# Kernel optimization log

Measured on AMD Instinct MI355X. Metric: run time of the kernel, lower is better.

Reference implementation:

```python
import jax, jax.numpy as jnp
import numpy as np

N_NODES = 50000
N_EDGES = 640000
D_IN = 128
HIDDEN = 128
OUT = 64


def sage_conv(x, edge_index, W_l, b_l, W_r):
    # PyG SAGEConv (mean aggr): out = lin_l(mean_j x_j) + lin_r(x_i)
    src, dst = edge_index[0], edge_index[1]
    msgs = x[src]                                             # [E, d] gather
    agg = jax.ops.segment_sum(msgs, dst, num_segments=x.shape[0])
    cnt = jax.ops.segment_sum(jnp.ones((edge_index.shape[1],), x.dtype), dst,
                              num_segments=x.shape[0])
    mean = agg / jnp.maximum(cnt, 1.0)[:, None]
    return mean @ W_l.T + b_l + x @ W_r.T


def setup_inputs() -> dict:
    key = jax.random.key(0)
    ks = jax.random.split(key, 8)
    s = lambda d: 1.0 / np.sqrt(d)
    x = jax.random.normal(ks[0], (N_NODES, D_IN), dtype=jnp.float32)
    edge_index = jax.random.randint(ks[1], (2, N_EDGES), 0, N_NODES, dtype=jnp.int64)
    return {
        "x": x,
        "edge_index": edge_index,
        "W1_l": jax.random.normal(ks[2], (HIDDEN, D_IN), jnp.float32) * s(D_IN),
        "b1_l": jnp.zeros((HIDDEN,), jnp.float32),
        "W1_r": jax.random.normal(ks[3], (HIDDEN, D_IN), jnp.float32) * s(D_IN),
        "W2_l": jax.random.normal(ks[4], (HIDDEN, HIDDEN), jnp.float32) * s(HIDDEN),
        "b2_l": jnp.zeros((HIDDEN,), jnp.float32),
        "W2_r": jax.random.normal(ks[5], (HIDDEN, HIDDEN), jnp.float32) * s(HIDDEN),
        "W3": jax.random.normal(ks[6], (OUT, HIDDEN), jnp.float32) * s(HIDDEN),
        "b3": jnp.zeros((OUT,), jnp.float32),
    }


def reference(x, edge_index, W1_l, b1_l, W1_r, W2_l, b2_l, W2_r, W3, b3):
    h = jax.nn.relu(sage_conv(x, edge_index, W1_l, b1_l, W1_r))
    h = jax.nn.relu(sage_conv(h, edge_index, W2_l, b2_l, W2_r))
    return h @ W3.T + b3
```

## Files before the change

### kernel.cpp

```cpp
#include <hip/hip_runtime.h>
#include <hip/hip_fp16.h>


typedef _Float16 f16x8 __attribute__((ext_vector_type(8)));
typedef float floatx4 __attribute__((ext_vector_type(4)));
typedef float floatx2 __attribute__((ext_vector_type(2)));

__device__ __forceinline__ unsigned short f2h(float f) {
    __half h = __float2half_rn(f);
    union { __half h; unsigned short s; } c; c.h = h; return c.s;
}
__device__ __forceinline__ __half2 u2h(unsigned u) {
    union { unsigned u; __half2 h; } c; c.u = u; return c.h;
}
__device__ __forceinline__ unsigned h2u(__half2 h) {
    union { __half2 h; unsigned u; } c; c.h = h; return c.u;
}
__device__ __forceinline__ __half2 shx(__half2 v, int m) {
    return u2h((unsigned)__shfl_xor((int)h2u(v), m, 64));
}
__device__ __forceinline__ ushort4 cvt4h(float4 v) {
    ushort4 o;
    o.x = f2h(v.x); o.y = f2h(v.y); o.z = f2h(v.z); o.w = f2h(v.w);
    return o;
}
__device__ __forceinline__ unsigned char f2fp8(float v) {
    return (unsigned char)(__builtin_amdgcn_cvt_pk_fp8_f32(v, v, 0, false) & 0xff);
}

#define WSEG 18432
__global__ __launch_bounds__(256) void prologue_kernel(
    const float* __restrict__ W1l, const float* __restrict__ W1r,
    const float* __restrict__ W2l, const float* __restrict__ W2r,
    const float* __restrict__ W3,  const float* __restrict__ x,
    unsigned short* __restrict__ wb,
    unsigned short* __restrict__ xb,
    unsigned char* __restrict__ x8,
    int* __restrict__ deg, int NX4, int ND4)
{
    int i = blockIdx.x * 256 + threadIdx.x;
    if (i < WSEG) {
        const float* s; int l;
        if (i < 8192)       { if (i < 4096) { s = W1l; l = i; }
                              else          { s = W1r; l = i - 4096; } }
        else if (i < 16384) { if (i < 12288){ s = W2l; l = i - 8192; }
                              else          { s = W2r; l = i - 12288; } }
        else                { s = W3; l = i - 16384; }
        ((ushort4*)wb)[i] = cvt4h(((const float4*)s)[l]);
        return;
    }
    int j = i - WSEG;
    if (j < NX4) {
        float4 v = ((const float4*)x)[j];
        ((ushort4*)xb)[j] = cvt4h(v);
        unsigned u8 = __builtin_amdgcn_cvt_pk_fp8_f32(v.x, v.y, 0, false);
        u8 = __builtin_amdgcn_cvt_pk_fp8_f32(v.z, v.w, u8, true);
        ((unsigned*)x8)[j] = u8;
        return;
    }
    int k = j - NX4;
    if (k < ND4) ((int4*)deg)[k] = make_int4(0, 0, 0, 0);
}

__global__ __launch_bounds__(256) void hist_kernel(const int* __restrict__ dst,
                                                   int* __restrict__ deg, int E) {
    int e = blockIdx.x * 256 + threadIdx.x;
    if (e < E) atomicAdd(deg + dst[e], 1);
}

__global__ __launch_bounds__(256) void scan_partial_kernel(
    const int* __restrict__ deg, int* __restrict__ partials, int N)
{
    __shared__ int ws[4];
    const int t = threadIdx.x, lane = t & 63, wave = t >> 6;
    const int i4 = blockIdx.x * 256 + t;
    const int n4 = (N + 3) / 4;
    int s = 0;
    if (i4 < n4) {
        int b = i4 * 4;
        if (b + 3 < N) {
            int4 v = ((const int4*)deg)[i4];
            s = v.x + v.y + v.z + v.w;
        } else {
            for (int q = 0; q < 4 && b + q < N; ++q) s += deg[b + q];
        }
    }
#pragma unroll
    for (int off = 32; off > 0; off >>= 1) s += __shfl_xor(s, off, 64);
    if (lane == 0) ws[wave] = s;
    __syncthreads();
    if (t == 0) partials[blockIdx.x] = ws[0] + ws[1] + ws[2] + ws[3];
}

__global__ __launch_bounds__(256) void scan_apply_kernel(
    const int* __restrict__ deg, const int* __restrict__ partials,
    int* __restrict__ rowptr, int* __restrict__ cursor, int N, int P)
{
    __shared__ int woff[4];
    __shared__ int s_base;
    const int t = threadIdx.x, lane = t & 63, wave = t >> 6;
    const int i4 = blockIdx.x * 256 + t;
    const int n4 = (N + 3) / 4;
    const int b = i4 * 4;

    if (wave == 0) {
        int v = (lane < P && lane < (int)blockIdx.x) ? partials[lane] : 0;
#pragma unroll
        for (int off = 32; off > 0; off >>= 1) v += __shfl_xor(v, off, 64);
        if (lane == 0) s_base = v;
    }

    int4 v = make_int4(0, 0, 0, 0);
    if (i4 < n4) {
        if (b + 3 < N) v = ((const int4*)deg)[i4];
        else {
            if (b + 0 < N) v.x = deg[b + 0];
            if (b + 1 < N) v.y = deg[b + 1];
            if (b + 2 < N) v.z = deg[b + 2];
        }
    }
    const int p1 = v.x, p2 = v.x + v.y, p3 = v.x + v.y + v.z;
    const int tsum = p3 + v.w;
    int incl = tsum;
#pragma unroll
    for (int off = 1; off < 64; off <<= 1) {
        int tt = __shfl_up(incl, off, 64);
        if (lane >= off) incl += tt;
    }
    const int texcl = incl - tsum;
    if (lane == 63) woff[wave] = incl;
    __syncthreads();
    int wo = 0;
#pragma unroll
    for (int w = 0; w < 4; ++w) if (w < wave) wo += woff[w];
    const int e = s_base + wo + texcl;
    if (blockIdx.x == 0 && t == 0) rowptr[0] = 0;
    if (b + 3 < N) {
        ((int4*)cursor)[i4] = make_int4(e, e + p1, e + p2, e + p3);
        rowptr[b + 1] = e + p1;
        rowptr[b + 2] = e + p2;
        rowptr[b + 3] = e + p3;
        rowptr[b + 4] = e + tsum;
    } else if (b < N) {
        if (b + 0 < N) { cursor[b + 0] = e;      rowptr[b + 1] = e + p1; }
        if (b + 1 < N) { cursor[b + 1] = e + p1; rowptr[b + 2] = e + p2; }
        if (b + 2 < N) { cursor[b + 2] = e + p2; rowptr[b + 3] = e + p3; }
    }
}

__global__ __launch_bounds__(256) void fill_kernel(const int* __restrict__ src,
                                                   const int* __restrict__ dst,
                                                   int* __restrict__ cursor,
                                                   int* __restrict__ csr, int E) {
    int e = blockIdx.x * 256 + threadIdx.x;
    if (e >= E) return;
    int pos = atomicAdd(cursor + dst[e], 1);
    csr[pos] = src[e];
}

template <bool WFP8, bool HEAD>
__global__ __launch_bounds__(256) void sage_layer_kernel(
    const unsigned short* __restrict__ feat,
    const unsigned char* __restrict__ feat8,
    const int* __restrict__ rowptr, const int* __restrict__ csr,
    const unsigned short* __restrict__ Wl,
    const unsigned short* __restrict__ Wr,
    const float* __restrict__ bias,
    unsigned short* __restrict__ out,
    unsigned char* __restrict__ out8,
    const unsigned short* __restrict__ W3,
    const float* __restrict__ b3,
    float* __restrict__ outF,
    int N)
{
    __shared__ unsigned short smean[16][136];
    __shared__ unsigned short sh2[HEAD ? 16 : 1][136];
    const int wave = threadIdx.x >> 6;
    const int lane = threadIdx.x & 63;
    const int r0 = blockIdx.x * 16;

    {
        const int grp = lane >> 4;
        const int col = lane & 15;
        const unsigned char* fq = feat8 + col * 8;

        int w[5];
#pragma unroll
        for (int q = 0; q < 5; ++q) {
            int n = r0 + wave * 4 + q;
            w[q] = rowptr[n < N ? n : N];
        }

        auto consume = [&](int mi, int beg, int end, uint2 pay[4]) {
            const int deg = end - beg;
            floatx2 a0 = (floatx2)(0.f), a1 = (floatx2)(0.f);
            floatx2 a2 = (floatx2)(0.f), a3 = (floatx2)(0.f);
#pragma unroll
            for (int c = 0; c < 4; ++c) {
                const int j = beg + grp + c * 4;
                const unsigned m = (j < end) ? 0xffffffffu : 0u;
                uint2 p = pay[c];
                p.x &= m; p.y &= m;
                a0 += __builtin_amdgcn_cvt_pk_f32_fp8(p.x, false);
                a1 += __builtin_amdgcn_cvt_pk_f32_fp8(p.x, true);
                a2 += __builtin_amdgcn_cvt_pk_f32_fp8(p.y, false);
                a3 += __builtin_amdgcn_cvt_pk_f32_fp8(p.y, true);
            }
            for (int jA = beg + 16 + grp; jA < end; jA += 16) {
                const int jB = jA + 4, jC = jA + 8, jD = jA + 12;
                const unsigned mB = (jB < end) ? 0xffffffffu : 0u;
                const unsigned mC = (jC < end) ? 0xffffffffu : 0u;
                const unsigned mD = (jD < end) ? 0xffffffffu : 0u;
                const int iA = csr[jA];
                const int iB = csr[mB ? jB : beg];
                const int iC = csr[mC ? jC : beg];
                const int iD = csr[mD ? jD : beg];
                uint2 pA = *(const uint2*)(fq + (size_t)iA * 128);
                uint2 pB = *(const uint2*)(fq + (size_t)iB * 128);
                uint2 pC = *(const uint2*)(fq + (size_t)iC * 128);
                uint2 pD = *(const uint2*)(fq + (size_t)iD * 128);
                pB.x &= mB; pB.y &= mB;
                pC.x &= mC; pC.y &= mC;
                pD.x &= mD; pD.y &= mD;
                a0 += __builtin_amdgcn_cvt_pk_f32_fp8(pA.x, false);
                a1 += __builtin_amdgcn_cvt_pk_f32_fp8(pA.x, true);
                a2 += __builtin_amdgcn_cvt_pk_f32_fp8(pA.y, false);
                a3 += __builtin_amdgcn_cvt_pk_f32_fp8(pA.y, true);
                a0 += __builtin_amdgcn_cvt_pk_f32_fp8(pB.x, false);
                a1 += __builtin_amdgcn_cvt_pk_f32_fp8(pB.x, true);
                a2 += __builtin_amdgcn_cvt_pk_f32_fp8(pB.y, false);
                a3 += __builtin_amdgcn_cvt_pk_f32_fp8(pB.y, true);
                a0 += __builtin_amdgcn_cvt_pk_f32_fp8(pC.x, false);
                a1 += __builtin_amdgcn_cvt_pk_f32_fp8(pC.x, true);
                a2 += __builtin_amdgcn_cvt_pk_f32_fp8(pC.y, false);
                a3 += __builtin_amdgcn_cvt_pk_f32_fp8(pC.y, true);
                a0 += __builtin_amdgcn_cvt_pk_f32_fp8(pD.x, false);
                a1 += __builtin_amdgcn_cvt_pk_f32_fp8(pD.x, true);
                a2 += __builtin_amdgcn_cvt_pk_f32_fp8(pD.y, false);
                a3 += __builtin_amdgcn_cvt_pk_f32_fp8(pD.y, true);
            }
            __half2 c0 = __floats2half2_rn(a0.x, a0.y);
            __half2 c1 = __floats2half2_rn(a1.x, a1.y);
            __half2 c2 = __floats2half2_rn(a2.x, a2.y);
            __half2 c3 = __floats2half2_rn(a3.x, a3.y);
            c0 = __hadd2(c0, shx(c0, 16)); c0 = __hadd2(c0, shx(c0, 32));
            c1 = __hadd2(c1, shx(c1, 16)); c1 = __hadd2(c1, shx(c1, 32));
            c2 = __hadd2(c2, shx(c2, 16)); c2 = __hadd2(c2, shx(c2, 32));
            c3 = __hadd2(c3, shx(c3, 16)); c3 = __hadd2(c3, shx(c3, 32));
            if (grp == 0) {
                const float inv = (deg > 0) ? 1.0f / (float)deg : 0.0f;
                uint4 o;
                o.x = h2u(__floats2half2_rn(__low2float(c0) * inv,
                                            __high2float(c0) * inv));
                o.y = h2u(__floats2half2_rn(__low2float(c1) * inv,
                                            __high2float(c1) * inv));
                o.z = h2u(__floats2half2_rn(__low2float(c2) * inv,
                                            __high2float(c2) * inv));
                o.w = h2u(__floats2half2_rn(__low2float(c3) * inv,
                                            __high2float(c3) * inv));
                *(uint4*)&smean[mi][col * 8] = o;
            }
        };

        int idx[4][4];
#pragma unroll
        for (int q = 0; q < 4; ++q) {
            const int beg = w[q], end = w[q + 1];
#pragma unroll
            for (int c = 0; c < 4; ++c) {
                const int j = beg + grp + c * 4;
                idx[q][c] = csr[j < end ? j : 0];
            }
        }
        __builtin_amdgcn_sched_barrier(0);
        uint2 pay[4][4];
#pragma unroll
        for (int q = 0; q < 4; ++q) {
#pragma unroll
            for (int c = 0; c < 4; ++c)
                pay[q][c] = *(const uint2*)(fq + (size_t)idx[q][c] * 128);
        }
        __builtin_amdgcn_sched_barrier(0);
#pragma unroll
        for (int q = 0; q < 4; ++q)
            consume(wave * 4 + q, w[q], w[q + 1], pay[q]);
    }
    __syncthreads();

    const int mrow = lane & 15;
    const int quad = lane >> 4;
    int selfRow = r0 + mrow;
    if (selfRow >= N) selfRow = N - 1;
    const size_t rowS = (size_t)selfRow * 128;

    floatx4 acc0 = (floatx4)(0.0f), acc1 = (floatx4)(0.0f);
    const int t0 = wave * 2, t1 = wave * 2 + 1;

#pragma unroll
    for (int kk = 0; kk < 4; ++kk) {
        const int k = kk * 32 + quad * 8;
        f16x8 aA = *(const f16x8*)&smean[mrow][k];
        f16x8 aS = *(const f16x8*)(feat + rowS + k);
        f16x8 bl0 = *(const f16x8*)(Wl + (size_t)(t0 * 16 + mrow) * 128 + k);
        acc0 = __builtin_amdgcn_mfma_f32_16x16x32_f16(aA, bl0, acc0, 0, 0, 0);
        f16x8 br0 = *(const f16x8*)(Wr + (size_t)(t0 * 16 + mrow) * 128 + k);
        acc0 = __builtin_amdgcn_mfma_f32_16x16x32_f16(aS, br0, acc0, 0, 0, 0);
        f16x8 bl1 = *(const f16x8*)(Wl + (size_t)(t1 * 16 + mrow) * 128 + k);
        acc1 = __builtin_amdgcn_mfma_f32_16x16x32_f16(aA, bl1, acc1, 0, 0, 0);
        f16x8 br1 = *(const f16x8*)(Wr + (size_t)(t1 * 16 + mrow) * 128 + k);
        acc1 = __builtin_amdgcn_mfma_f32_16x16x32_f16(aS, br1, acc1, 0, 0, 0);
    }

    const float b0 = bias[t0 * 16 + mrow];
    const float b1 = bias[t1 * 16 + mrow];
#pragma unroll
    for (int i = 0; i < 4; ++i) {
        const int r = r0 + quad * 4 + i;
        const float v0 = fmaxf(acc0[i] + b0, 0.0f);
        const float v1 = fmaxf(acc1[i] + b1, 0.0f);
        if (HEAD) {
            sh2[quad * 4 + i][t0 * 16 + mrow] = f2h(v0);
            sh2[quad * 4 + i][t1 * 16 + mrow] = f2h(v1);
        } else if (r < N) {
            out[(size_t)r * 128 + t0 * 16 + mrow] = f2h(v0);
            out[(size_t)r * 128 + t1 * 16 + mrow] = f2h(v1);
            if (WFP8) {
                out8[(size_t)r * 128 + t0 * 16 + mrow] = f2fp8(v0);
                out8[(size_t)r * 128 + t1 * 16 + mrow] = f2fp8(v1);
            }
        }
    }

    if (HEAD) {
        __syncthreads();
        floatx4 ah = (floatx4)(0.0f);
#pragma unroll
        for (int kk = 0; kk < 4; ++kk) {
            const int k = kk * 32 + quad * 8;
            f16x8 aA = *(const f16x8*)&sh2[mrow][k];
            f16x8 b = *(const f16x8*)(W3 + (size_t)(wave * 16 + mrow) * 128 + k);
            ah = __builtin_amdgcn_mfma_f32_16x16x32_f16(aA, b, ah, 0, 0, 0);
        }
        const float bh = b3[wave * 16 + mrow];
#pragma unroll
        for (int i = 0; i < 4; ++i) {
            const int r = r0 + quad * 4 + i;
            if (r < N)
                outF[(size_t)r * 64 + wave * 16 + mrow] = ah[i] + bh;
        }
    }
}

extern "C" void kernel_launch(void* const* d_in, const int* in_sizes, int n_in,
                              void* d_out, int out_size, void* d_ws, size_t ws_size,
                              hipStream_t stream)
{
    const float* x   = (const float*)d_in[0];
    const int* ei    = (const int*)d_in[1];
    const float* W1l = (const float*)d_in[2];
    const float* b1l = (const float*)d_in[3];
    const float* W1r = (const float*)d_in[4];
    const float* W2l = (const float*)d_in[5];
    const float* b2l = (const float*)d_in[6];
    const float* W2r = (const float*)d_in[7];
    const float* W3  = (const float*)d_in[8];
    const float* b3  = (const float*)d_in[9];
    float* out = (float*)d_out;

    const int N = in_sizes[0] / 128;
    const int E = in_sizes[1] / 2;
    const int* src = ei;
    const int* dst = ei + E;

    const int n4 = (N + 3) / 4;
    int* deg_i    = (int*)d_ws;
    int* partials = deg_i + n4 * 4;
    int* rowptr   = partials + 64;
    int* cursor   = rowptr + N + 4;
    int* csr      = cursor + n4 * 4;
    unsigned short* xb   = (unsigned short*)(csr + E);
    unsigned short* h1   = xb + (size_t)N * 128;
    unsigned short* wb1l = h1 + (size_t)N * 128;
    unsigned short* wb1r = wb1l + 16384;
    unsigned short* wb2l = wb1r + 16384;
    unsigned short* wb2r = wb2l + 16384;
    unsigned short* wb3  = wb2r + 16384;
    unsigned char* x8    = (unsigned char*)(wb3 + 8192);
    unsigned char* h18   = x8 + (size_t)N * 128;

    const int lblk = (N + 15) / 16;
    const int eblk = (E + 255) / 256;
    const int NX4  = N * 32;
    const int P    = (n4 + 255) / 256;

    {
        int total = WSEG + NX4 + n4;
        hipLaunchKernelGGL(prologue_kernel, dim3((total + 255) / 256), dim3(256), 0,
                           stream, W1l, W1r, W2l, W2r, W3, x, wb1l, xb, x8, deg_i,
                           NX4, n4);
    }

    hipLaunchKernelGGL(hist_kernel, dim3(eblk), dim3(256), 0, stream, dst, deg_i, E);
    hipLaunchKernelGGL(scan_partial_kernel, dim3(P), dim3(256), 0, stream,
                       deg_i, partials, N);
    hipLaunchKernelGGL(scan_apply_kernel, dim3(P), dim3(256), 0, stream,
                       deg_i, partials, rowptr, cursor, N, P);
    hipLaunchKernelGGL(fill_kernel, dim3(eblk), dim3(256), 0, stream,
                       src, dst, cursor, csr, E);

    hipLaunchKernelGGL((sage_layer_kernel<true, false>), dim3(lblk), dim3(256), 0,
                       stream, xb, x8, rowptr, csr, wb1l, wb1r, b1l,
                       h1, h18, nullptr, nullptr, nullptr, N);
    hipLaunchKernelGGL((sage_layer_kernel<false, true>), dim3(lblk), dim3(256), 0,
                       stream, h1, h18, rowptr, csr, wb2l, wb2r, b2l,
                       nullptr, nullptr, wb3, b3, out, N);
}
```

Before: 261.2 us.

## Stage first-window neighbor gathers into LDS via global_load_lds

Result: slower. 266.5 us (+2.0%).

```diff
diff --git a/kernel.cpp b/kernel.cpp
--- a/kernel.cpp
+++ b/kernel.cpp
@@ -26,6 +26,11 @@
 }
 __device__ __forceinline__ unsigned char f2fp8(float v) {
     return (unsigned char)(__builtin_amdgcn_cvt_pk_fp8_f32(v, v, 0, false) & 0xff);
+}
+__device__ __forceinline__ void gld_lds16(const void* g, void* l) {
+    __builtin_amdgcn_global_load_lds(
+        (const __attribute__((address_space(1))) void*)g,
+        (__attribute__((address_space(3))) void*)l, 16, 0, 0);
 }
 
 #define WSEG 18432
@@ -173,8 +178,10 @@
     float* __restrict__ outF,
     int N)
 {
+    __shared__ __align__(16) unsigned char swin[32768];
     __shared__ unsigned short smean[16][136];
-    __shared__ unsigned short sh2[HEAD ? 16 : 1][136];
+    unsigned short (*sh2)[136] = (unsigned short (*)[136])swin;
+
     const int wave = threadIdx.x >> 6;
     const int lane = threadIdx.x & 63;
     const int r0 = blockIdx.x * 16;
@@ -191,15 +198,38 @@
             w[q] = rowptr[n < N ? n : N];
         }
 
-        auto consume = [&](int mi, int beg, int end, uint2 pay[4]) {
+        {
+            const int ql = lane >> 4, rl = lane & 15;
+            const int begL = (ql == 0) ? w[0] : (ql == 1) ? w[1]
+                           : (ql == 2) ? w[2] : w[3];
+            const int endL = (ql == 0) ? w[1] : (ql == 1) ? w[2]
+                           : (ql == 2) ? w[3] : w[4];
+            const int j = begL + rl;
+            const int idxv = csr[(j < endL) ? j : 0];
+
+            unsigned char* wbase = swin + wave * 8192;
+            const int sub = lane >> 3;
+            const int byt = (lane & 7) * 16;
+#pragma unroll
+            for (int i = 0; i < 8; ++i) {
+                const int rowidx = __shfl(idxv, i * 8 + sub, 64);
+                gld_lds16(feat8 + (size_t)rowidx * 128 + byt,
+                          wbase + i * 1024);
+            }
+        }
+        asm volatile("s_waitcnt vmcnt(0)" ::: "memory");
+        __builtin_amdgcn_sched_barrier(0);
+
+        auto consume = [&](int mi, int q, int beg, int end) {
             const int deg = end - beg;
+            const unsigned char* base = swin + wave * 8192 + q * 2048;
             floatx2 a0 = (floatx2)(0.f), a1 = (floatx2)(0.f);
             floatx2 a2 = (floatx2)(0.f), a3 = (floatx2)(0.f);
 #pragma unroll
             for (int c = 0; c < 4; ++c) {
                 const int j = beg + grp + c * 4;
                 const unsigned m = (j < end) ? 0xffffffffu : 0u;
-                uint2 p = pay[c];
+                uint2 p = *(const uint2*)(base + (grp + c * 4) * 128 + col * 8);
                 p.x &= m; p.y &= m;
                 a0 += __builtin_amdgcn_cvt_pk_f32_fp8(p.x, false);
                 a1 += __builtin_amdgcn_cvt_pk_f32_fp8(p.x, true);
@@ -262,28 +292,9 @@
             }
         };
 
-        int idx[4][4];
-#pragma unroll
-        for (int q = 0; q < 4; ++q) {
-            const int beg = w[q], end = w[q + 1];
-#pragma unroll
-            for (int c = 0; c < 4; ++c) {
-                const int j = beg + grp + c * 4;
-                idx[q][c] = csr[j < end ? j : 0];
-            }
-        }
-        __builtin_amdgcn_sched_barrier(0);
-        uint2 pay[4][4];
-#pragma unroll
-        for (int q = 0; q < 4; ++q) {
-#pragma unroll
-            for (int c = 0; c < 4; ++c)
-                pay[q][c] = *(const uint2*)(fq + (size_t)idx[q][c] * 128);
-        }
-        __builtin_amdgcn_sched_barrier(0);
 #pragma unroll
         for (int q = 0; q < 4; ++q)
-            consume(wave * 4 + q, w[q], w[q + 1], pay[q]);
+            consume(wave * 4 + q, q, w[q], w[q + 1]);
     }
     __syncthreads();
 
```
